# Optimization experiments

Measured on AMD Instinct MI355X. Metric: run time of the kernel, lower is better.

Reference implementation:

```python
import math
import jax, jax.numpy as jnp
import numpy as np

NEG = -1e10


def _rope_cos_sin(T, head_dim, dtype):
    # theta_i = 10000^(-2*(i-1)/dim), i=1..dim/2  ->  j=0..dim/2-1: 10000^(-2j/dim)
    j = jnp.arange(head_dim // 2, dtype=jnp.float32)
    inv_freq = 1.0 / (10000.0 ** (2.0 * j / head_dim))
    t = jnp.arange(T, dtype=jnp.float32)
    ang = t[:, None] * inv_freq[None, :]          # [T, hd/2]
    return jnp.cos(ang).astype(dtype), jnp.sin(ang).astype(dtype)


def _apply_rope(x, cos, sin):
    # x: [B, H, T, hd]; complex multiply (cos + i sin) * (x0 + i x1)
    B, H, T, hd = x.shape
    xr = x.reshape(B, H, T, hd // 2, 2)
    x0, x1 = xr[..., 0], xr[..., 1]
    c = cos[None, None]  # [1,1,T,hd/2]
    s = sin[None, None]
    o0 = c * x0 - s * x1
    o1 = s * x0 + c * x1
    return jnp.stack([o0, o1], axis=-1).reshape(B, H, T, hd)


def setup_inputs() -> dict:
    key = jax.random.key(0)
    ks = jax.random.split(key, 9)
    B, T, C = 2, 2048, 1024
    std = 0.02
    return {
        "x": jax.random.normal(ks[0], (B, T, C), jnp.float32),
        "Wq": jax.random.normal(ks[1], (C, C), jnp.float32) * std,
        "bq": jnp.zeros((C,), jnp.float32),
        "Wk": jax.random.normal(ks[2], (C, C), jnp.float32) * std,
        "bk": jnp.zeros((C,), jnp.float32),
        "Wv": jax.random.normal(ks[3], (C, C), jnp.float32) * std,
        "bv": jnp.zeros((C,), jnp.float32),
        "Wp": jax.random.normal(ks[4], (C, C), jnp.float32) * std,
        "bp": jnp.zeros((C,), jnp.float32),
    }


def reference(x, Wq, bq, Wk, bk, Wv, bv, Wp, bp):
    B, T, C = x.shape
    H = 16
    hd = C // H

    def heads(y):  # [B,T,C] -> [B,H,T,hd]
        return y.reshape(B, T, H, hd).transpose(0, 2, 1, 3)

    q = heads(x @ Wq.T + bq)
    k = heads(x @ Wk.T + bk)
    v = heads(x @ Wv.T + bv)

    cos, sin = _rope_cos_sin(T, hd, x.dtype)
    q = _apply_rope(q, cos, sin)
    k = _apply_rope(k, cos, sin)

    att = jnp.einsum('bhqd,bhkd->bhqk', q, k) * (1.0 / math.sqrt(hd))
    causal = jnp.tril(jnp.ones((T, T), bool))
    att = jnp.where(causal[None, None], att, jnp.asarray(NEG, att.dtype))
    att = jax.nn.softmax(att, axis=-1)

    y = jnp.einsum('bhqk,bhkd->bhqd', att, v)
    y = y.transpose(0, 2, 1, 3).reshape(B, T, C)
    return y @ Wp.T + bp
```

## Files before the change

kernel.cpp:

```cpp
#include <hip/hip_runtime.h>
#include <math.h>

typedef unsigned short u16;
typedef unsigned int u32;
typedef unsigned long long u64;
typedef __attribute__((ext_vector_type(8))) short short8;
typedef __attribute__((ext_vector_type(4))) float f32x4;
typedef __attribute__((ext_vector_type(4))) u16 u16x4;
typedef __attribute__((ext_vector_type(4))) u32 u32x4;

#define AS1 __attribute__((address_space(1)))
#define AS3 __attribute__((address_space(3)))

#define QSCALE 0.18033688011112042f

__device__ __forceinline__ u16 f2bf(float f) {
  union { float f; u32 i; } u; u.f = f;
  u32 r = u.i + 0x7FFFu + ((u.i >> 16) & 1u);
  return (u16)(r >> 16);
}

__device__ __forceinline__ u32 pk_bf16(float a, float b) {
  u32 r;
  asm volatile("v_cvt_pk_bf16_f32 %0, %1, %2" : "=v"(r) : "v"(a), "v"(b));
  return r;
}

__device__ __forceinline__ void gl_lds16(const void* g, void* l) {
  __builtin_amdgcn_global_load_lds((const AS1 u32*)g, (AS3 u32*)l, 16, 0, 0);
}

#define MFMA32(a, b, c) __builtin_amdgcn_mfma_f32_16x16x32_bf16(a, b, c, 0, 0, 0)

__global__ void cvt_all(const float* __restrict__ x,
                        const float* __restrict__ Wq, const float* __restrict__ Wk,
                        const float* __restrict__ Wv, const float* __restrict__ Wp,
                        u16* __restrict__ xb,
                        u16* __restrict__ Wqb, u16* __restrict__ Wkb,
                        u16* __restrict__ Wvb, u16* __restrict__ Wpb,
                        float* __restrict__ cosT, float* __restrict__ sinT,
                        int n4x, int n4tot) {
  int i = blockIdx.x * 256 + threadIdx.x;
  if (i >= n4tot) {
    int k = i - n4tot;
    int t = k >> 5, j = k & 31;
    float inv = powf(10000.0f, -(float)j / 32.0f);
    float ang = (float)t * inv;
    cosT[k] = cosf(ang);
    sinT[k] = sinf(ang);
    return;
  }
  const float* src; u16* dst; int off;
  if (i < n4x) { src = x; dst = xb; off = i; }
  else {
    int wi = i - n4x;
    int sel = wi >> 18;
    off = wi & ((1 << 18) - 1);
    src = sel == 0 ? Wq : sel == 1 ? Wk : sel == 2 ? Wv : Wp;
    dst = sel == 0 ? Wqb : sel == 1 ? Wkb : sel == 2 ? Wvb : Wpb;
  }
  float4 v = ((const float4*)src)[off];
  u16x4 o = { f2bf(v.x), f2bf(v.y), f2bf(v.z), f2bf(v.w) };
  ((u16x4*)dst)[off] = o;
}

__global__ __launch_bounds__(256, 2) void gemm_qkv(
    const u16* __restrict__ xb,
    const u16* __restrict__ Wqb, const u16* __restrict__ Wkb, const u16* __restrict__ Wvb,
    const float* __restrict__ bq, const float* __restrict__ bk, const float* __restrict__ bv,
    const float* __restrict__ cosT, const float* __restrict__ sinT,
    u16* __restrict__ Qb, u16* __restrict__ Kb, u16* __restrict__ Vb) {
  const int K = 1024, N = 1024;
  __shared__ __attribute__((aligned(16))) u16 As[128 * 64];
  __shared__ __attribute__((aligned(16))) u16 Bs[128 * 64];
  const int tid = threadIdx.x;
  const int lane = tid & 63;
  const int hi = lane >> 4, cc = lane & 15;
  const int w = tid >> 6, wm = w >> 1, wn = w & 1;

  const int lin = blockIdx.x + 24 * blockIdx.y;
  const int a_ = lin & 7;
  const int m_ = lin >> 3;
  const int c_ = a_ * 3 + (m_ % 3);
  const int sel = c_ >> 3;
  const int row0 = (m_ / 3) * 128, col0 = (c_ & 7) * 128;

  const u16* W = sel == 0 ? Wqb : sel == 1 ? Wkb : Wvb;
  const float* bias = sel == 0 ? bq : sel == 1 ? bk : bv;
  u16* Out = sel == 0 ? Qb : sel == 1 ? Kb : Vb;

  const int lr = tid >> 3;
  const int lkb = (((tid & 7) ^ (lr & 7)) * 8);
  const u16* Ag = xb + (size_t)(row0 + lr) * K + lkb;
  const u16* Wg = W + (size_t)(col0 + lr) * K + lkb;

  f32x4 acc[4][4];
#pragma unroll
  for (int m = 0; m < 4; ++m)
#pragma unroll
    for (int n = 0; n < 4; ++n) acc[m][n] = f32x4{0.f, 0.f, 0.f, 0.f};

  for (int k0 = 0; k0 < K; k0 += 64) {
    __syncthreads();
#pragma unroll
    for (int j = 0; j < 4; ++j) {
      gl_lds16(Ag + (size_t)j * 32 * K + k0, As + j * 2048 + tid * 8);
      gl_lds16(Wg + (size_t)j * 32 * K + k0, Bs + j * 2048 + tid * 8);
    }
    __syncthreads();
    short8 a[2][4], b[2][4];
#pragma unroll
    for (int kk = 0; kk < 2; ++kk) {
#pragma unroll
      for (int m = 0; m < 4; ++m)
        a[kk][m] = *(const short8*)(As + (wm * 64 + m * 16 + cc) * 64 +
                                    (((kk * 4 + hi) ^ (cc & 7)) * 8));
#pragma unroll
      for (int n = 0; n < 4; ++n)
        b[kk][n] = *(const short8*)(Bs + (wn * 64 + n * 16 + cc) * 64 +
                                    (((kk * 4 + hi) ^ (cc & 7)) * 8));
    }
#pragma unroll
    for (int kk = 0; kk < 2; ++kk)
#pragma unroll
      for (int m = 0; m < 4; ++m)
#pragma unroll
        for (int n = 0; n < 4; ++n)
          acc[m][n] = MFMA32(a[kk][m], b[kk][n], acc[m][n]);
  }

  if (sel < 2) {
    const float qs = (sel == 0) ? QSCALE : 1.0f;
#pragma unroll
    for (int n = 0; n < 4; ++n) {
      const int col = col0 + wn * 64 + n * 16 + cc;
      const int j = (col & 63) >> 1;
      const float bb = bias[col];
#pragma unroll
      for (int m = 0; m < 4; ++m) {
        const int rw = row0 + wm * 64 + m * 16 + hi * 4;
#pragma unroll
        for (int r = 0; r < 4; ++r) {
          const int row = rw + r;
          const int t = row & 2047;
          float v = acc[m][n][r] + bb;
          float pv = __shfl_xor(v, 1);
          float c = cosT[t * 32 + j], s = sinT[t * 32 + j];
          float oo = (cc & 1) ? (s * pv + c * v) : (c * v - s * pv);
          Out[(size_t)row * N + col] = f2bf(oo * qs);
        }
      }
    }
  } else {
#pragma unroll
    for (int n = 0; n < 4; ++n) {
      const int col = col0 + wn * 64 + n * 16 + cc;
      const float bb = bias[col];
#pragma unroll
      for (int m = 0; m < 4; ++m) {
        const int rw = row0 + wm * 64 + m * 16 + hi * 4;
#pragma unroll
        for (int r = 0; r < 4; ++r)
          Out[(size_t)(rw + r) * N + col] = f2bf(acc[m][n][r] + bb);
      }
    }
  }
}

__global__ __launch_bounds__(256, 2) void flash_mfma(
    const u16* __restrict__ Qb, const u16* __restrict__ Kb,
    const u16* __restrict__ Vb, u16* __restrict__ Yb) {
  const int T = 2048, C = 1024;
  __shared__ __attribute__((aligned(16))) u16 Ks[64 * 64];
  __shared__ __attribute__((aligned(16))) u16 Vt[64 * 64];
  __shared__ __attribute__((aligned(16))) u16 Ps[4][2][16 * 64];

  const int tid = threadIdx.x;
  const int lane = tid & 63;
  const int hi = lane >> 4, cc = lane & 15;
  const int hi4 = hi * 4;
  const int w = tid >> 6;

  const int lin = blockIdx.x + 16 * blockIdx.y;
  const int bh  = (lin & 7) * 4 + ((lin >> 3) & 3);
  const int qtA = lin >> 5;
  const int qtB = 31 - qtA;
  const size_t hbase = (size_t)(bh >> 4) * T * C + (size_t)(bh & 15) * 64;
  const int qA0w = qtA * 64 + w * 16;
  const int qB0w = qtB * 64 + w * 16;

  short8 qaA0, qaA1, qaB0, qaB1;
  {
    const u16* qp = Qb + hbase + (size_t)(qA0w + cc) * C + hi * 8;
    qaA0 = *(const short8*)qp;
    qaA1 = *(const short8*)(qp + 32);
    qp = Qb + hbase + (size_t)(qB0w + cc) * C + hi * 8;
    qaB0 = *(const short8*)qp;
    qaB1 = *(const short8*)(qp + 32);
  }

  f32x4 oA[4], oB[4];
#pragma unroll
  for (int nt = 0; nt < 4; ++nt) {
    oA[nt] = f32x4{0.f, 0.f, 0.f, 0.f};
    oB[nt] = f32x4{0.f, 0.f, 0.f, 0.f};
  }
  float mA = -1e30f, lA = 0.f, mB = -1e30f, lB = 0.f;

  const int krow = tid >> 2, kcol = (tid & 3) * 16;
  const int vd0 = (tid & 31) * 2, vkey0 = (tid >> 5) * 8;
  const u16* kgp = Kb + hbase + (size_t)krow * C + kcol;
  const u16* vgp = Vb + hbase + (size_t)vkey0 * C + vd0;

  short8 kr0, kr1;
  u32 vr_[8];

  auto LOADT = [&](int kt) {
    const size_t off = (size_t)(kt * 64) * C;
    kr0 = *(const short8*)(kgp + off);
    kr1 = *(const short8*)(kgp + off + 8);
#pragma unroll
    for (int j = 0; j < 8; ++j)
      vr_[j] = *(const u32*)(vgp + off + (size_t)j * C);
  };

  char* KsB = (char*)Ks;
  char* VtB = (char*)Vt;
  char* PsA_ = (char*)(Ps[w][0]);
  char* PsB_ = (char*)(Ps[w][1]);

  auto WRITET = [&]() {
    const int kb = krow * 128 + kcol * 2;
    const int ksw = (krow & 7) << 4;
    *(short8*)(KsB + (kb ^ ksw)) = kr0;
    *(short8*)(KsB + ((kb + 16) ^ ksw)) = kr1;
    u32 lo0 = (vr_[0] & 0xFFFFu) | (vr_[1] << 16);
    u32 lo1 = (vr_[2] & 0xFFFFu) | (vr_[3] << 16);
    u32 lo2 = (vr_[4] & 0xFFFFu) | (vr_[5] << 16);
    u32 lo3 = (vr_[6] & 0xFFFFu) | (vr_[7] << 16);
    u32 hh0 = (vr_[0] >> 16) | (vr_[1] & 0xFFFF0000u);
    u32 hh1 = (vr_[2] >> 16) | (vr_[3] & 0xFFFF0000u);
    u32 hh2 = (vr_[4] >> 16) | (vr_[5] & 0xFFFF0000u);
    u32 hh3 = (vr_[6] >> 16) | (vr_[7] & 0xFFFF0000u);
    const int d1 = vd0 + 1;
    u32x4 vlo = {lo0, lo1, lo2, lo3};
    u32x4 vhi = {hh0, hh1, hh2, hh3};
    *(u32x4*)(VtB + ((vd0 * 128 + vkey0 * 2) ^ ((vd0 & 7) << 4))) = vlo;
    *(u32x4*)(VtB + ((d1 * 128 + vkey0 * 2) ^ ((d1 & 7) << 4))) = vhi;
  };

  const int ksw2 = (cc & 7) << 4;

  auto QKT = [&](short8 (&kf)[4][2], const short8& qa0, const short8& qa1,
                 f32x4 (&s)[4]) {
#pragma unroll
    for (int nt = 0; nt < 4; ++nt) {
      f32x4 z = f32x4{0.f, 0.f, 0.f, 0.f};
      z = MFMA32(kf[nt][0], qa0, z);
      z = MFMA32(kf[nt][1], qa1, z);
      s[nt] = z;
    }
  };

  auto SM = [&](f32x4 (&s)[4], float& mrow, float& lsum, f32x4* o, char* PsX) {
    float tm = s[0][0];
#pragma unroll
    for (int nt = 0; nt < 4; ++nt)
#pragma unroll
      for (int r = 0; r < 4; ++r) tm = fmaxf(tm, s[nt][r]);
    tm = fmaxf(tm, __shfl_xor(tm, 16));
    tm = fmaxf(tm, __shfl_xor(tm, 32));
    const bool need = tm > mrow + 8.0f;
    float corr = 1.0f;
    if (need) { corr = exp2f(mrow - tm); mrow = tm; }
    float psum = 0.f;
#pragma unroll
    for (int nt = 0; nt < 4; ++nt) {
      float e0 = exp2f(s[nt][0] - mrow);
      float e1 = exp2f(s[nt][1] - mrow);
      float e2 = exp2f(s[nt][2] - mrow);
      float e3 = exp2f(s[nt][3] - mrow);
      psum += (e0 + e1) + (e2 + e3);
      u32 pr[2] = { pk_bf16(e0, e1), pk_bf16(e2, e3) };
      *(u64*)(PsX + ((cc * 128 + nt * 32 + hi * 8) ^ ksw2)) = *(const u64*)pr;
    }
    psum += __shfl_xor(psum, 16);
    psum += __shfl_xor(psum, 32);
    lsum = lsum * corr + psum;
    if (__any(need)) {
#pragma unroll
      for (int nt = 0; nt < 4; ++nt) o[nt] *= corr;
    }
  };

  auto MASK = [&](f32x4 (&s)[4]) {
    const int qloc = w * 16 + cc;
#pragma unroll
    for (int nt = 0; nt < 4; ++nt)
#pragma unroll
      for (int r = 0; r < 4; ++r)
        if (nt * 16 + hi4 + r > qloc) s[nt][r] = -1e30f;
  };

  LOADT(0);
  WRITET();
  LOADT(1);
  __syncthreads();

  for (int kt = 0; kt <= qtB; ++kt) {
    short8 kf[4][2];
#pragma unroll
    for (int nt = 0; nt < 4; ++nt) {
      const int kb = (nt * 16 + cc) * 128 + hi * 16;
      kf[nt][0] = *(const short8*)(KsB + (kb ^ ksw2));
      kf[nt][1] = *(const short8*)(KsB + ((kb + 64) ^ ksw2));
    }

    const bool actA = (kt <= qtA);
    f32x4 sB[4], sA[4];
    QKT(kf, qaB0, qaB1, sB);
    if (actA) QKT(kf, qaA0, qaA1, sA);
    if (kt == qtB) MASK(sB);
    if (actA && kt == qtA) MASK(sA);

    SM(sB, mB, lB, oB, PsB_);
    if (actA) SM(sA, mA, lA, oA, PsA_);

    short8 vf[2][4];
#pragma unroll
    for (int kc = 0; kc < 2; ++kc)
#pragma unroll
      for (int nt = 0; nt < 4; ++nt)
        vf[kc][nt] = *(const short8*)(VtB + (((nt * 16 + cc) * 128 + kc * 64 + hi * 16) ^ ksw2));

#pragma unroll
    for (int kc = 0; kc < 2; ++kc) {
      short8 pa = *(const short8*)(PsB_ + ((cc * 128 + kc * 64 + hi * 16) ^ ksw2));
#pragma unroll
      for (int nt = 0; nt < 4; ++nt)
        oB[nt] = MFMA32(vf[kc][nt], pa, oB[nt]);
    }
    if (actA) {
#pragma unroll
      for (int kc = 0; kc < 2; ++kc) {
        short8 pa = *(const short8*)(PsA_ + ((cc * 128 + kc * 64 + hi * 16) ^ ksw2));
#pragma unroll
        for (int nt = 0; nt < 4; ++nt)
          oA[nt] = MFMA32(vf[kc][nt], pa, oA[nt]);
      }
    }

    if (kt < qtB) {
      __syncthreads();
      WRITET();
      if (kt + 1 < qtB) LOADT(kt + 2);
      __syncthreads();
    }
  }

  const float ivA = 1.0f / lA, ivB = 1.0f / lB;
#pragma unroll
  for (int nt = 0; nt < 4; ++nt) {
    u16x4 yA = { f2bf(oA[nt][0] * ivA), f2bf(oA[nt][1] * ivA),
                 f2bf(oA[nt][2] * ivA), f2bf(oA[nt][3] * ivA) };
    *(u16x4*)(Yb + hbase + (size_t)(qA0w + cc) * C + nt * 16 + hi4) = yA;
    u16x4 yB = { f2bf(oB[nt][0] * ivB), f2bf(oB[nt][1] * ivB),
                 f2bf(oB[nt][2] * ivB), f2bf(oB[nt][3] * ivB) };
    *(u16x4*)(Yb + hbase + (size_t)(qB0w + cc) * C + nt * 16 + hi4) = yB;
  }
}

__global__ __launch_bounds__(256, 2) void gemm_proj(
    const u16* __restrict__ A, const u16* __restrict__ W,
    const float* __restrict__ bias, float* __restrict__ Out) {
  const int K = 1024, N = 1024;
  __shared__ __attribute__((aligned(16))) u16 As[128 * 64];
  __shared__ __attribute__((aligned(16))) u16 Bs[64 * 64];
  const int tid = threadIdx.x;
  const int lane = tid & 63;
  const int hi = lane >> 4, cc = lane & 15;
  const int w = tid >> 6, wm = w >> 1, wn = w & 1;

  const int lin = blockIdx.x + 16 * blockIdx.y;
  const int colt = (lin & 7) * 2 + ((lin >> 3) & 1);
  const int row0 = (lin >> 4) * 128, col0 = colt * 64;

  const int lr = tid >> 3;
  const int lkb = (((tid & 7) ^ (lr & 7)) * 8);
  const u16* Ag = A + (size_t)(row0 + lr) * K + lkb;
  const u16* Wg = W + (size_t)(col0 + lr) * K + lkb;

  f32x4 acc[4][2];
#pragma unroll
  for (int m = 0; m < 4; ++m)
#pragma unroll
    for (int n = 0; n < 2; ++n) acc[m][n] = f32x4{0.f, 0.f, 0.f, 0.f};

  for (int k0 = 0; k0 < K; k0 += 64) {
    __syncthreads();
#pragma unroll
    for (int j = 0; j < 4; ++j)
      gl_lds16(Ag + (size_t)j * 32 * K + k0, As + j * 2048 + tid * 8);
#pragma unroll
    for (int j = 0; j < 2; ++j)
      gl_lds16(Wg + (size_t)j * 32 * K + k0, Bs + j * 2048 + tid * 8);
    __syncthreads();
    short8 a[2][4], b[2][2];
#pragma unroll
    for (int kk = 0; kk < 2; ++kk) {
#pragma unroll
      for (int m = 0; m < 4; ++m)
        a[kk][m] = *(const short8*)(As + (wm * 64 + m * 16 + cc) * 64 +
                                    (((kk * 4 + hi) ^ (cc & 7)) * 8));
#pragma unroll
      for (int n = 0; n < 2; ++n)
        b[kk][n] = *(const short8*)(Bs + (wn * 32 + n * 16 + cc) * 64 +
                                    (((kk * 4 + hi) ^ (cc & 7)) * 8));
    }
#pragma unroll
    for (int kk = 0; kk < 2; ++kk)
#pragma unroll
      for (int m = 0; m < 4; ++m)
#pragma unroll
        for (int n = 0; n < 2; ++n)
          acc[m][n] = MFMA32(a[kk][m], b[kk][n], acc[m][n]);
  }

#pragma unroll
  for (int n = 0; n < 2; ++n) {
    const int col = col0 + wn * 32 + n * 16 + cc;
    const float bb = bias[col];
#pragma unroll
    for (int m = 0; m < 4; ++m) {
      const int rw = row0 + wm * 64 + m * 16 + hi * 4;
#pragma unroll
      for (int r = 0; r < 4; ++r)
        Out[(size_t)(rw + r) * N + col] = acc[m][n][r] + bb;
    }
  }
}

extern "C" void kernel_launch(void* const* d_in, const int* in_sizes, int n_in,
                              void* d_out, int out_size, void* d_ws, size_t ws_size,
                              hipStream_t stream) {
  const float* x  = (const float*)d_in[0];
  const float* Wq = (const float*)d_in[1];
  const float* bq = (const float*)d_in[2];
  const float* Wk = (const float*)d_in[3];
  const float* bk = (const float*)d_in[4];
  const float* Wv = (const float*)d_in[5];
  const float* bv = (const float*)d_in[6];
  const float* Wp = (const float*)d_in[7];
  const float* bp = (const float*)d_in[8];
  float* out = (float*)d_out;

  const int B = 2, T = 2048, C = 1024;
  const int M = B * T;
  const size_t MC = (size_t)M * C;
  const size_t CC = (size_t)C * C;

  char* p = (char*)d_ws;
  u16* xb  = (u16*)p;  p += MC * 2;
  u16* Wqb = (u16*)p;  p += CC * 2;
  u16* Wkb = (u16*)p;  p += CC * 2;
  u16* Wvb = (u16*)p;  p += CC * 2;
  u16* Wpb = (u16*)p;  p += CC * 2;
  u16* Qbb = (u16*)p;  p += MC * 2;
  u16* Kbb = (u16*)p;  p += MC * 2;
  u16* Vbb = (u16*)p;  p += MC * 2;
  float* cosT = (float*)p; p += (size_t)T * 32 * 4;
  float* sinT = (float*)p; p += (size_t)T * 32 * 4;

  const int n4x = (int)(MC / 4);
  const int n4tot = n4x + 4 * (int)(CC / 4);
  const int ntot = n4tot + T * 32;
  cvt_all<<<(ntot + 255) / 256, 256, 0, stream>>>(x, Wq, Wk, Wv, Wp,
                                                  xb, Wqb, Wkb, Wvb, Wpb,
                                                  cosT, sinT, n4x, n4tot);

  dim3 gq(24, M / 128);
  gemm_qkv<<<gq, 256, 0, stream>>>(xb, Wqb, Wkb, Wvb, bq, bk, bv, cosT, sinT, Qbb, Kbb, Vbb);

  dim3 fg(16, B * 16);
  flash_mfma<<<fg, 256, 0, stream>>>(Qbb, Kbb, Vbb, xb);

  dim3 gp(C / 64, M / 128);
  gemm_proj<<<gp, 256, 0, stream>>>(xb, Wpb, bp, out);
}
```

Baseline: 123.5 us.

## Shrink flash blocks to 32 query rows with 2 waves, doubling grid size

The attention kernel now uses 128-thread blocks that each own two 32-row query chunks (paired from the front and back of the sequence for causal balance), launched as 1024 blocks instead of 512. Each thread loads twice as much K/V per tile, and the P scratch buffer is shared between the A and B passes, so softmax and PV now run back to back per pass. Smaller blocks are meant to raise occupancy and balance load, at the cost of loading each K/V tile from global memory for fewer query rows. The QKV GEMM launch bound is also raised to 3 blocks per CU, which may force register spilling.

```diff
diff --git a/kernel.cpp b/kernel.cpp
--- a/kernel.cpp
+++ b/kernel.cpp
@@ -64,7 +64,7 @@
   ((u16x4*)dst)[off] = o;
 }
 
-__global__ __launch_bounds__(256, 2) void gemm_qkv(
+__global__ __launch_bounds__(256, 3) void gemm_qkv(
     const u16* __restrict__ xb,
     const u16* __restrict__ Wqb, const u16* __restrict__ Wkb, const u16* __restrict__ Wvb,
     const float* __restrict__ bq, const float* __restrict__ bk, const float* __restrict__ bv,
@@ -167,13 +167,13 @@
   }
 }
 
-__global__ __launch_bounds__(256, 2) void flash_mfma(
+__global__ __launch_bounds__(128, 4) void flash_mfma(
     const u16* __restrict__ Qb, const u16* __restrict__ Kb,
     const u16* __restrict__ Vb, u16* __restrict__ Yb) {
   const int T = 2048, C = 1024;
   __shared__ __attribute__((aligned(16))) u16 Ks[64 * 64];
   __shared__ __attribute__((aligned(16))) u16 Vt[64 * 64];
-  __shared__ __attribute__((aligned(16))) u16 Ps[4][2][16 * 64];
+  __shared__ __attribute__((aligned(16))) u16 Ps[2][16 * 64];
 
   const int tid = threadIdx.x;
   const int lane = tid & 63;
@@ -181,13 +181,16 @@
   const int hi4 = hi * 4;
   const int w = tid >> 6;
 
-  const int lin = blockIdx.x + 16 * blockIdx.y;
-  const int bh  = (lin & 7) * 4 + ((lin >> 3) & 3);
-  const int qtA = lin >> 5;
-  const int qtB = 31 - qtA;
+  const int lin = blockIdx.x;
+  const int bh = (lin & 7) * 4 + ((lin >> 3) & 3);
+  const int x = lin >> 5;
+  const int cA = x, cB = 63 - x;
+  const int diagA = cA >> 1, diagB = cB >> 1;
   const size_t hbase = (size_t)(bh >> 4) * T * C + (size_t)(bh & 15) * 64;
-  const int qA0w = qtA * 64 + w * 16;
-  const int qB0w = qtB * 64 + w * 16;
+  const int qA0w = cA * 32 + w * 16;
+  const int qB0w = cB * 32 + w * 16;
+  const int qlocA = (cA & 1) * 32 + w * 16 + cc;
+  const int qlocB = (cB & 1) * 32 + w * 16 + cc;
 
   short8 qaA0, qaA1, qaB0, qaB1;
   {
@@ -207,46 +210,54 @@
   }
   float mA = -1e30f, lA = 0.f, mB = -1e30f, lB = 0.f;
 
-  const int krow = tid >> 2, kcol = (tid & 3) * 16;
-  const int vd0 = (tid & 31) * 2, vkey0 = (tid >> 5) * 8;
-  const u16* kgp = Kb + hbase + (size_t)krow * C + kcol;
+  const int krow = tid >> 1, kcolu = (tid & 1) * 32;
+  const int vd0 = (tid & 31) * 2, vkey0 = (tid >> 5) * 16;
+  const u16* kgp = Kb + hbase + (size_t)krow * C + kcolu;
   const u16* vgp = Vb + hbase + (size_t)vkey0 * C + vd0;
 
-  short8 kr0, kr1;
-  u32 vr_[8];
+  short8 kr_[4];
+  u32 vr_[16];
 
   auto LOADT = [&](int kt) {
     const size_t off = (size_t)(kt * 64) * C;
-    kr0 = *(const short8*)(kgp + off);
-    kr1 = *(const short8*)(kgp + off + 8);
-#pragma unroll
-    for (int j = 0; j < 8; ++j)
+#pragma unroll
+    for (int j = 0; j < 4; ++j)
+      kr_[j] = *(const short8*)(kgp + off + j * 8);
+#pragma unroll
+    for (int j = 0; j < 16; ++j)
       vr_[j] = *(const u32*)(vgp + off + (size_t)j * C);
   };
 
   char* KsB = (char*)Ks;
   char* VtB = (char*)Vt;
-  char* PsA_ = (char*)(Ps[w][0]);
-  char* PsB_ = (char*)(Ps[w][1]);
+  char* PsW = (char*)(Ps[w]);
 
   auto WRITET = [&]() {
-    const int kb = krow * 128 + kcol * 2;
+    const int kbse = krow * 128 + kcolu * 2;
     const int ksw = (krow & 7) << 4;
-    *(short8*)(KsB + (kb ^ ksw)) = kr0;
-    *(short8*)(KsB + ((kb + 16) ^ ksw)) = kr1;
-    u32 lo0 = (vr_[0] & 0xFFFFu) | (vr_[1] << 16);
-    u32 lo1 = (vr_[2] & 0xFFFFu) | (vr_[3] << 16);
-    u32 lo2 = (vr_[4] & 0xFFFFu) | (vr_[5] << 16);
-    u32 lo3 = (vr_[6] & 0xFFFFu) | (vr_[7] << 16);
-    u32 hh0 = (vr_[0] >> 16) | (vr_[1] & 0xFFFF0000u);
-    u32 hh1 = (vr_[2] >> 16) | (vr_[3] & 0xFFFF0000u);
-    u32 hh2 = (vr_[4] >> 16) | (vr_[5] & 0xFFFF0000u);
-    u32 hh3 = (vr_[6] >> 16) | (vr_[7] & 0xFFFF0000u);
+#pragma unroll
+    for (int j = 0; j < 4; ++j)
+      *(short8*)(KsB + ((kbse + j * 16) ^ ksw)) = kr_[j];
     const int d1 = vd0 + 1;
-    u32x4 vlo = {lo0, lo1, lo2, lo3};
-    u32x4 vhi = {hh0, hh1, hh2, hh3};
-    *(u32x4*)(VtB + ((vd0 * 128 + vkey0 * 2) ^ ((vd0 & 7) << 4))) = vlo;
-    *(u32x4*)(VtB + ((d1 * 128 + vkey0 * 2) ^ ((d1 & 7) << 4))) = vhi;
+    const int sw0 = (vd0 & 7) << 4;
+    const int sw1 = (d1 & 7) << 4;
+#pragma unroll
+    for (int g = 0; g < 2; ++g) {
+      const u32* v8 = vr_ + g * 8;
+      u32 lo0 = (v8[0] & 0xFFFFu) | (v8[1] << 16);
+      u32 lo1 = (v8[2] & 0xFFFFu) | (v8[3] << 16);
+      u32 lo2 = (v8[4] & 0xFFFFu) | (v8[5] << 16);
+      u32 lo3 = (v8[6] & 0xFFFFu) | (v8[7] << 16);
+      u32 hh0 = (v8[0] >> 16) | (v8[1] & 0xFFFF0000u);
+      u32 hh1 = (v8[2] >> 16) | (v8[3] & 0xFFFF0000u);
+      u32 hh2 = (v8[4] >> 16) | (v8[5] & 0xFFFF0000u);
+      u32 hh3 = (v8[6] >> 16) | (v8[7] & 0xFFFF0000u);
+      u32x4 vlo = {lo0, lo1, lo2, lo3};
+      u32x4 vhi = {hh0, hh1, hh2, hh3};
+      const int kb = (vkey0 + g * 8) * 2;
+      *(u32x4*)(VtB + ((vd0 * 128 + kb) ^ sw0)) = vlo;
+      *(u32x4*)(VtB + ((d1 * 128 + kb) ^ sw1)) = vhi;
+    }
   };
 
   const int ksw2 = (cc & 7) << 4;
@@ -262,7 +273,7 @@
     }
   };
 
-  auto SM = [&](f32x4 (&s)[4], float& mrow, float& lsum, f32x4* o, char* PsX) {
+  auto SM = [&](f32x4 (&s)[4], float& mrow, float& lsum, f32x4* o) {
     float tm = s[0][0];
 #pragma unroll
     for (int nt = 0; nt < 4; ++nt)
@@ -282,7 +293,7 @@
       float e3 = exp2f(s[nt][3] - mrow);
       psum += (e0 + e1) + (e2 + e3);
       u32 pr[2] = { pk_bf16(e0, e1), pk_bf16(e2, e3) };
-      *(u64*)(PsX + ((cc * 128 + nt * 32 + hi * 8) ^ ksw2)) = *(const u64*)pr;
+      *(u64*)(PsW + ((cc * 128 + nt * 32 + hi * 8) ^ ksw2)) = *(const u64*)pr;
     }
     psum += __shfl_xor(psum, 16);
     psum += __shfl_xor(psum, 32);
@@ -293,13 +304,22 @@
     }
   };
 
-  auto MASK = [&](f32x4 (&s)[4]) {
-    const int qloc = w * 16 + cc;
+  auto MASK = [&](f32x4 (&s)[4], int qloc) {
 #pragma unroll
     for (int nt = 0; nt < 4; ++nt)
 #pragma unroll
       for (int r = 0; r < 4; ++r)
         if (nt * 16 + hi4 + r > qloc) s[nt][r] = -1e30f;
+  };
+
+  auto PV = [&](short8 (&vf)[2][4], f32x4* o) {
+#pragma unroll
+    for (int kc = 0; kc < 2; ++kc) {
+      short8 pa = *(const short8*)(PsW + ((cc * 128 + kc * 64 + hi * 16) ^ ksw2));
+#pragma unroll
+      for (int nt = 0; nt < 4; ++nt)
+        o[nt] = MFMA32(vf[kc][nt], pa, o[nt]);
+    }
   };
 
   LOADT(0);
@@ -307,7 +327,7 @@
   LOADT(1);
   __syncthreads();
 
-  for (int kt = 0; kt <= qtB; ++kt) {
+  for (int kt = 0; kt <= diagB; ++kt) {
     short8 kf[4][2];
 #pragma unroll
     for (int nt = 0; nt < 4; ++nt) {
@@ -316,15 +336,12 @@
       kf[nt][1] = *(const short8*)(KsB + ((kb + 64) ^ ksw2));
     }
 
-    const bool actA = (kt <= qtA);
+    const bool actA = (kt <= diagA);
     f32x4 sB[4], sA[4];
     QKT(kf, qaB0, qaB1, sB);
     if (actA) QKT(kf, qaA0, qaA1, sA);
-    if (kt == qtB) MASK(sB);
-    if (actA && kt == qtA) MASK(sA);
-
-    SM(sB, mB, lB, oB, PsB_);
-    if (actA) SM(sA, mA, lA, oA, PsA_);
+    if (kt == diagB) MASK(sB, qlocB);
+    if (actA && kt == diagA) MASK(sA, qlocA);
 
     short8 vf[2][4];
 #pragma unroll
@@ -333,27 +350,17 @@
       for (int nt = 0; nt < 4; ++nt)
         vf[kc][nt] = *(const short8*)(VtB + (((nt * 16 + cc) * 128 + kc * 64 + hi * 16) ^ ksw2));
 
-#pragma unroll
-    for (int kc = 0; kc < 2; ++kc) {
-      short8 pa = *(const short8*)(PsB_ + ((cc * 128 + kc * 64 + hi * 16) ^ ksw2));
-#pragma unroll
-      for (int nt = 0; nt < 4; ++nt)
-        oB[nt] = MFMA32(vf[kc][nt], pa, oB[nt]);
-    }
+    SM(sB, mB, lB, oB);
+    PV(vf, oB);
     if (actA) {
-#pragma unroll
-      for (int kc = 0; kc < 2; ++kc) {
-        short8 pa = *(const short8*)(PsA_ + ((cc * 128 + kc * 64 + hi * 16) ^ ksw2));
-#pragma unroll
-        for (int nt = 0; nt < 4; ++nt)
-          oA[nt] = MFMA32(vf[kc][nt], pa, oA[nt]);
-      }
-    }
-
-    if (kt < qtB) {
+      SM(sA, mA, lA, oA);
+      PV(vf, oA);
+    }
+
+    if (kt < diagB) {
       __syncthreads();
       WRITET();
-      if (kt + 1 < qtB) LOADT(kt + 2);
+      if (kt + 1 < diagB) LOADT(kt + 2);
       __syncthreads();
     }
   }
@@ -481,8 +488,7 @@
   dim3 gq(24, M / 128);
   gemm_qkv<<<gq, 256, 0, stream>>>(xb, Wqb, Wkb, Wvb, bq, bk, bv, cosT, sinT, Qbb, Kbb, Vbb);
 
-  dim3 fg(16, B * 16);
-  flash_mfma<<<fg, 256, 0, stream>>>(Qbb, Kbb, Vbb, xb);
+  flash_mfma<<<1024, 128, 0, stream>>>(Qbb, Kbb, Vbb, xb);
 
   dim3 gp(C / 64, M / 128);
   gemm_proj<<<gp, 256, 0, stream>>>(xb, Wpb, bp, out);
```

Measured after the change: 336.1 us. 172% more time.
